# Kernel tuning notes

Hardware: AMD Instinct MI355X
Metric: run time of the kernel (lower is better)

The kernel has to match this reference:

```python
import jax, jax.numpy as jnp
import numpy as np

N_HEADS = 16
MAX_LEN = 4096
D_MODEL = 1024
EPS = 1e-6


def setup_inputs() -> dict:
    key = jax.random.key(0)
    ks = jax.random.split(key, 12)
    B, L, D = 4, 4096, D_MODEL
    s = 1.0 / np.sqrt(D)
    inp = {
        "q": jax.random.normal(ks[0], (B, L, D), jnp.float32),
        "k": jax.random.normal(ks[1], (B, L, D), jnp.float32),
        "v": jax.random.normal(ks[2], (B, L, D), jnp.float32),
        "Wq": jax.random.normal(ks[3], (D, D), jnp.float32) * s,
        "bq": jax.random.normal(ks[4], (D,), jnp.float32) * s,
        "Wk": jax.random.normal(ks[5], (D, D), jnp.float32) * s,
        "bk": jax.random.normal(ks[6], (D,), jnp.float32) * s,
        "Wv": jax.random.normal(ks[7], (D, D), jnp.float32) * s,
        "bv": jax.random.normal(ks[8], (D,), jnp.float32) * s,
        "Wo": jax.random.normal(ks[9], (D, D), jnp.float32) * s,
        "bo": jax.random.normal(ks[10], (D,), jnp.float32) * s,
    }
    return inp


def _cos_attn(q, k, v, Wq, bq, Wk, bk, Wv, bv, Wo, bo):
    B, Lq, D = q.shape
    Lk = k.shape[1]
    H = N_HEADS
    hd = D // H
    # torch Linear: x @ W^T + b
    qh = (q @ Wq.T + bq).reshape(B, Lq, H, hd).transpose(0, 2, 1, 3)  # b h l d
    kh = (k @ Wk.T + bk).reshape(B, Lk, H, hd).transpose(0, 2, 1, 3)
    vh = (v @ Wv.T + bv).reshape(B, Lk, H, hd).transpose(0, 2, 1, 3)
    qh = jax.nn.relu(qh)
    kh = jax.nn.relu(kh)
    # weight_index buffer: pi*(1..max_len)/(2*max_len), shape (1,1,L,1)
    idx = (np.pi * jnp.arange(1, MAX_LEN + 1, dtype=jnp.float32) / (2 * MAX_LEN))
    qi = idx[:Lq][None, None, :, None]
    ki = idx[:Lk][None, None, :, None]
    q_ = jnp.concatenate([qh * jnp.sin(qi), qh * jnp.cos(qi)], axis=-1)  # b h l 2d
    k_ = jnp.concatenate([kh * jnp.sin(ki), kh * jnp.cos(ki)], axis=-1)
    kv_ = jnp.einsum("bnld,bnlm->bndm", k_, vh)  # b h 2d d
    z_ = 1.0 / jnp.maximum(jnp.einsum("bnld,bnd->bnl", q_, jnp.sum(k_, axis=2)), EPS)
    attn = jnp.einsum("bnld,bndm,bnl->bnlm", q_, kv_, z_)  # b h l d
    attn = attn.transpose(0, 2, 1, 3).reshape(B, Lq, D)
    return attn @ Wo.T + bo  # dropout: eval mode (identity)


def reference(q, k, v, Wq, bq, Wk, bk, Wv, bv, Wo, bo):
    return _cos_attn(q, k, v, Wq, bq, Wk, bk, Wv, bv, Wo, bo)
```

## Files before the change

### kernel.cpp

```cpp
#include <hip/hip_runtime.h>

typedef __bf16 bf16x8 __attribute__((ext_vector_type(8)));
typedef float f32x4 __attribute__((ext_vector_type(4)));

#define PI_F 3.14159265358979323846f

__device__ __forceinline__ unsigned short f2bf(float f) {
  unsigned u = __builtin_bit_cast(unsigned, f);
  u += 0x7fffu + ((u >> 16) & 1u);
  return (unsigned short)(u >> 16);
}

__device__ __forceinline__ unsigned scale_pair(unsigned w, float f) {
  const float lo = __builtin_bit_cast(float, w << 16);
  const float hi = __builtin_bit_cast(float, w & 0xffff0000u);
  return (unsigned)f2bf(lo * f) | ((unsigned)f2bf(hi * f) << 16);
}

#define GLD16(gp, lp)                                          \
  __builtin_amdgcn_global_load_lds(                            \
      (const __attribute__((address_space(1))) void*)(gp),     \
      (__attribute__((address_space(3))) void*)(lp), 16, 0, 0)

struct AReg { float4 a0, a1, a2, a3, a4, a5, a6, a7; };

__device__ __forceinline__ uint4 cvtpk16(float4 x, float4 y) {
  unsigned c0, c1, c2, c3;
  asm("v_cvt_pk_bf16_f32 %0, %1, %2" : "=v"(c0) : "v"(x.x), "v"(x.y));
  asm("v_cvt_pk_bf16_f32 %0, %1, %2" : "=v"(c1) : "v"(x.z), "v"(x.w));
  asm("v_cvt_pk_bf16_f32 %0, %1, %2" : "=v"(c2) : "v"(y.x), "v"(y.y));
  asm("v_cvt_pk_bf16_f32 %0, %1, %2" : "=v"(c3) : "v"(y.z), "v"(y.w));
  uint4 u; u.x = c0; u.y = c1; u.z = c2; u.w = c3;
  return u;
}

__device__ __forceinline__ uint2 cvtpk8(float a, float b, float c, float d) {
  unsigned lo, hi;
  asm("v_cvt_pk_bf16_f32 %0, %1, %2" : "=v"(lo) : "v"(a), "v"(b));
  asm("v_cvt_pk_bf16_f32 %0, %1, %2" : "=v"(hi) : "v"(c), "v"(d));
  uint2 r; r.x = lo; r.y = hi;
  return r;
}

__device__ __forceinline__ void unpack8(uint4 w, float* f) {
  f[0] = __builtin_bit_cast(float, w.x << 16);
  f[1] = __builtin_bit_cast(float, w.x & 0xffff0000u);
  f[2] = __builtin_bit_cast(float, w.y << 16);
  f[3] = __builtin_bit_cast(float, w.y & 0xffff0000u);
  f[4] = __builtin_bit_cast(float, w.z << 16);
  f[5] = __builtin_bit_cast(float, w.z & 0xffff0000u);
  f[6] = __builtin_bit_cast(float, w.w << 16);
  f[7] = __builtin_bit_cast(float, w.w & 0xffff0000u);
}

__global__ __launch_bounds__(256) void convert_w(
    const float* __restrict__ Wq, const float* __restrict__ Wk,
    const float* __restrict__ Wv, const float* __restrict__ Wo,
    unsigned short* __restrict__ Wqb, unsigned short* __restrict__ Wkb,
    unsigned short* __restrict__ Wvb, unsigned short* __restrict__ Wob) {
  const int region = blockIdx.y;
  const float* s; unsigned short* d;
  switch (region) {
    case 0: s = Wq; d = Wqb; break;
    case 1: s = Wk; d = Wkb; break;
    case 2: s = Wv; d = Wvb; break;
    default: s = Wo; d = Wob; break;
  }
  const float4* s4 = (const float4*)s;
  ushort4* d4 = (ushort4*)d;
  const int n4 = 262144;
  for (int i = blockIdx.x * 256 + threadIdx.x; i < n4; i += gridDim.x * 256) {
    float4 f = s4[i];
    ushort4 o;
    o.x = f2bf(f.x); o.y = f2bf(f.y); o.z = f2bf(f.z); o.w = f2bf(f.w);
    d4[i] = o;
  }
}

template <int MODE>
__global__ __launch_bounds__(512, 2) void gemm256(
    const float* __restrict__ A32, const unsigned short* __restrict__ Bw,
    const float* __restrict__ bias, unsigned short* __restrict__ out) {
  constexpr int K = 1024, NKT = 16;
  __shared__ unsigned short S[81920];
  const int tid = threadIdx.x;
  const int wave = tid >> 6, lane = tid & 63;
  const int fr = lane & 15, fq = lane >> 4;
  const int wr = wave >> 2, wc = wave & 3;
  const int cpx = gridDim.x >> 3;
  const int wg = (blockIdx.x & 7) * cpx + (blockIdx.x >> 3);
  const int mt = wg >> 2, ntile = wg & 3;
  const int m0 = mt * 256, n0 = ntile * 256;

  const int srow = tid >> 3;
  const int ac16 = tid & 7;
  const int scolE = ((ac16 << 4) ^ ((srow & 7) << 4)) >> 1;
  const unsigned short* bSrc = Bw + (size_t)(n0 + srow) * K + scolE;
  const int awoff = (ac16 ^ (srow & 7)) << 3;
  AReg R;

#define BSTAGE(kt_, idx_) do {                                                     \
    const int kc_ = (kt_) * 64;                                                    \
    unsigned short* bb_ = S + 32768 + (idx_) * 16384 + wave * 512;                 \
    GLD16(bSrc + kc_, bb_);                                                        \
    GLD16(bSrc + (size_t)65536 + kc_, bb_ + 4096);                                 \
    GLD16(bSrc + (size_t)131072 + kc_, bb_ + 8192);                                \
    GLD16(bSrc + (size_t)196608 + kc_, bb_ + 12288);                               \
  } while (0)

#define ALOAD_ALL(kt_) do {                                                        \
    const int kc_ = (kt_) * 64;                                                    \
    const float4* p_;                                                              \
    p_ = (const float4*)(A32 + (size_t)(m0 + srow) * K + kc_) + ac16 * 2;          \
    R.a0 = p_[0]; R.a1 = p_[1];                                                    \
    p_ = (const float4*)(A32 + (size_t)(m0 + 64 + srow) * K + kc_) + ac16 * 2;     \
    R.a2 = p_[0]; R.a3 = p_[1];                                                    \
    p_ = (const float4*)(A32 + (size_t)(m0 + 128 + srow) * K + kc_) + ac16 * 2;    \
    R.a4 = p_[0]; R.a5 = p_[1];                                                    \
    p_ = (const float4*)(A32 + (size_t)(m0 + 192 + srow) * K + kc_) + ac16 * 2;    \
    R.a6 = p_[0]; R.a7 = p_[1];                                                    \
  } while (0)

#define AWRITE_ALL(idx_) do {                                                      \
    unsigned short* dst_ = &S[(idx_) * 16384 + srow * 64 + awoff];                 \
    *(uint4*)(dst_)         = cvtpk16(R.a0, R.a1);                                 \
    *(uint4*)(dst_ + 4096)  = cvtpk16(R.a2, R.a3);                                 \
    *(uint4*)(dst_ + 8192)  = cvtpk16(R.a4, R.a5);                                 \
    *(uint4*)(dst_ + 12288) = cvtpk16(R.a6, R.a7);                                 \
  } while (0)

  const int xorv = (fr & 7) << 4;
  const unsigned cbE0 = (unsigned)(((fq * 16) ^ xorv) >> 1);
  const unsigned cbE1 = (unsigned)(((64 + fq * 16) ^ xorv) >> 1);

  f32x4 acc[8][4] = {};
  ALOAD_ALL(0);
  BSTAGE(0, 0);
  BSTAGE(1, 1);
  AWRITE_ALL(0);
  ALOAD_ALL(1);
  asm volatile("s_waitcnt vmcnt(12) lgkmcnt(0)" ::: "memory");
  __builtin_amdgcn_s_barrier();

  for (int kt = 0; kt < NKT; ++kt) {
    const unsigned aB = (unsigned)((kt & 1) * 16384 + wr * 8192 + fr * 64);
    int bcur = kt % 3;
    const unsigned bB = (unsigned)(32768 + bcur * 16384 + (wc >> 1) * 8192 +
                                   ((wc & 1) * 64 + fr) * 64);
    bf16x8 af[4][2], b0[2][2], b1[2][2];
#pragma unroll
    for (int mm = 0; mm < 4; ++mm) {
      const unsigned r = aB + (unsigned)(mm * 1024);
      af[mm][0] = *(const bf16x8*)&S[r + cbE0];
      af[mm][1] = *(const bf16x8*)&S[r + cbE1];
    }
#pragma unroll
    for (int nn = 0; nn < 2; ++nn) {
      const unsigned r0 = bB + (unsigned)(nn * 1024);
      b0[nn][0] = *(const bf16x8*)&S[r0 + cbE0];
      b0[nn][1] = *(const bf16x8*)&S[r0 + cbE1];
      const unsigned r1 = bB + (unsigned)((2 + nn) * 1024);
      b1[nn][0] = *(const bf16x8*)&S[r1 + cbE0];
      b1[nn][1] = *(const bf16x8*)&S[r1 + cbE1];
    }
    if (kt + 2 < NKT) {
      int bst = bcur + 2; if (bst >= 3) bst -= 3;
      BSTAGE(kt + 2, bst);
    }
    __builtin_amdgcn_s_barrier();
    __builtin_amdgcn_s_setprio(1);
#pragma unroll
    for (int mm = 0; mm < 4; ++mm) {
#pragma unroll
      for (int nn = 0; nn < 2; ++nn) {
        acc[mm][nn] = __builtin_amdgcn_mfma_f32_16x16x32_bf16(af[mm][0], b0[nn][0], acc[mm][nn], 0, 0, 0);
        acc[mm][nn] = __builtin_amdgcn_mfma_f32_16x16x32_bf16(af[mm][1], b0[nn][1], acc[mm][nn], 0, 0, 0);
        acc[mm][2 + nn] = __builtin_amdgcn_mfma_f32_16x16x32_bf16(af[mm][0], b1[nn][0], acc[mm][2 + nn], 0, 0, 0);
        acc[mm][2 + nn] = __builtin_amdgcn_mfma_f32_16x16x32_bf16(af[mm][1], b1[nn][1], acc[mm][2 + nn], 0, 0, 0);
      }
    }
    __builtin_amdgcn_s_setprio(0);
    __builtin_amdgcn_s_barrier();
#pragma unroll
    for (int mm = 0; mm < 4; ++mm) {
      const unsigned r = aB + (unsigned)((4 + mm) * 1024);
      af[mm][0] = *(const bf16x8*)&S[r + cbE0];
      af[mm][1] = *(const bf16x8*)&S[r + cbE1];
    }
    if (kt + 1 < NKT) AWRITE_ALL((kt + 1) & 1);
    if (kt + 2 < NKT) ALOAD_ALL(kt + 2);
    __builtin_amdgcn_s_barrier();
    __builtin_amdgcn_s_setprio(1);
#pragma unroll
    for (int mm = 0; mm < 4; ++mm) {
#pragma unroll
      for (int nn = 0; nn < 2; ++nn) {
        acc[4 + mm][nn] = __builtin_amdgcn_mfma_f32_16x16x32_bf16(af[mm][0], b0[nn][0], acc[4 + mm][nn], 0, 0, 0);
        acc[4 + mm][nn] = __builtin_amdgcn_mfma_f32_16x16x32_bf16(af[mm][1], b0[nn][1], acc[4 + mm][nn], 0, 0, 0);
        acc[4 + mm][2 + nn] = __builtin_amdgcn_mfma_f32_16x16x32_bf16(af[mm][0], b1[nn][0], acc[4 + mm][2 + nn], 0, 0, 0);
        acc[4 + mm][2 + nn] = __builtin_amdgcn_mfma_f32_16x16x32_bf16(af[mm][1], b1[nn][1], acc[4 + mm][2 + nn], 0, 0, 0);
      }
    }
    __builtin_amdgcn_s_setprio(0);
    asm volatile("s_waitcnt lgkmcnt(0)" ::: "memory");
    __builtin_amdgcn_s_barrier();
  }
#undef BSTAGE
#undef ALOAD_ALL
#undef AWRITE_ALL

  const int colb = n0 + wc * 64 + fr;
  const int rtb0 = wr * 128 + fq * 4;
  const int mlo = m0 & 4095;
  const int b16 = (m0 >> 12) << 4;
  const int hbase = n0 >> 6;

  if constexpr (MODE == 0) {
    float bb4[4];
#pragma unroll
    for (int nq = 0; nq < 4; ++nq) bb4[nq] = bias[colb + nq * 16];
    __syncthreads();
#pragma unroll
    for (int mq = 0; mq < 8; ++mq) {
#pragma unroll
      for (int rr = 0; rr < 4; ++rr) {
        const int rt = rtb0 + mq * 16 + rr;
        const int e = (rt >> 2) & 7;
#pragma unroll
        for (int nq = 0; nq < 4; ++nq) {
          const int ct = wc * 64 + nq * 16 + fr;
          const int sct = (ct & 7) | ((((ct >> 3) ^ e) & 31) << 3);
          S[rt * 256 + sct] = f2bf(fmaxf(acc[mq][nq][rr] + bb4[nq], 0.0f));
        }
      }
    }
    __syncthreads();
#pragma unroll
    for (int it = 0; it < 16; ++it) {
      const int rt = it * 16 + (tid >> 5);
      const int co = tid & 31;
      const int chunk = co ^ ((rt >> 2) & 7);
      uint4 w = *(const uint4*)&S[rt * 256 + chunk * 8];
      const int h = hbase + (co >> 3);
      const size_t addr = ((size_t)(b16 + h) * 4096 + mlo + rt) * 64 + ((co & 7) << 3);
      *(uint4*)(out + addr) = w;
    }
  } else {
    float bb4[4];
#pragma unroll
    for (int nq = 0; nq < 4; ++nq) bb4[nq] = bias[colb + nq * 16];
#pragma unroll
    for (int mq = 0; mq < 8; ++mq)
#pragma unroll
      for (int nq = 0; nq < 4; ++nq)
#pragma unroll
        for (int rr = 0; rr < 4; ++rr) {
          float val = acc[mq][nq][rr] + bb4[nq];
          if constexpr (MODE == 5) val = fmaxf(val, 0.0f);
          acc[mq][nq][rr] = val;
        }
    __syncthreads();
#pragma unroll
    for (int mq = 0; mq < 8; ++mq) {
      const int rtb = rtb0 + mq * 16;
#pragma unroll
      for (int nq = 0; nq < 4; ++nq) {
        const int ct = wc * 64 + nq * 16 + fr;
        uint2 w = cvtpk8(acc[mq][nq][0], acc[mq][nq][1], acc[mq][nq][2], acc[mq][nq][3]);
        *(uint2*)&S[ct * 256 + (rtb ^ ((ct & 7) << 2))] = w;
      }
    }
    __syncthreads();
#pragma unroll
    for (int it = 0; it < 16; ++it) {
      const int ct = it * 16 + (tid >> 5);
      const int lo = (tid & 31) << 3;
      const int sw = (ct & 7) << 2;
      uint2 r0 = *(const uint2*)&S[ct * 256 + (lo ^ sw)];
      uint2 r1 = *(const uint2*)&S[ct * 256 + ((lo + 4) ^ sw)];
      uint4 w; w.x = r0.x; w.y = r0.y; w.z = r1.x; w.w = r1.y;
      const int h = hbase + (ct >> 6), dd = ct & 63;
      const size_t addr = ((size_t)(b16 + h) * 64 + dd) * 4096 + mlo + lo;
      *(uint4*)(out + addr) = w;
    }
  }
}

__global__ __launch_bounds__(512, 2) void gemm_o(
    const unsigned short* __restrict__ Ain, const unsigned short* __restrict__ Bw,
    const float* __restrict__ bias, unsigned short* __restrict__ out) {
  constexpr int K = 1024, NKT = 16;
  __shared__ unsigned short S[81920];
  const int tid = threadIdx.x;
  const int wave = tid >> 6, lane = tid & 63;
  const int fr = lane & 15, fq = lane >> 4;
  const int wr = wave >> 2, wc = wave & 3;
  const int wg = (blockIdx.x & 7) * 32 + (blockIdx.x >> 3);
  const int mt = wg >> 2, ntile = wg & 3;
  const int m0 = mt * 256, n0 = ntile * 256;

  const int srow = tid >> 3;
  const int ac16 = tid & 7;
  const int scolE = ((ac16 << 4) ^ ((srow & 7) << 4)) >> 1;
  const unsigned short* bSrc = Bw + (size_t)(n0 + srow) * K + scolE;
  const unsigned short* aSrcB = Ain + (size_t)(m0 + srow) * K + scolE;

#define BSTAGE(kt_, idx_) do {                                                     \
    const int kc_ = (kt_) * 64;                                                    \
    unsigned short* bb_ = S + 32768 + (idx_) * 16384 + wave * 512;                 \
    GLD16(bSrc + kc_, bb_);                                                        \
    GLD16(bSrc + (size_t)65536 + kc_, bb_ + 4096);                                 \
    GLD16(bSrc + (size_t)131072 + kc_, bb_ + 8192);                                \
    GLD16(bSrc + (size_t)196608 + kc_, bb_ + 12288);                               \
  } while (0)

#define ASTAGE(kt_, idx_) do {                                                     \
    const int kc_ = (kt_) * 64;                                                    \
    unsigned short* ab_ = S + (idx_) * 16384 + wave * 512;                         \
    GLD16(aSrcB + kc_, ab_);                                                       \
    GLD16(aSrcB + (size_t)65536 + kc_, ab_ + 4096);                                \
    GLD16(aSrcB + (size_t)131072 + kc_, ab_ + 8192);                               \
    GLD16(aSrcB + (size_t)196608 + kc_, ab_ + 12288);                              \
  } while (0)

  const int xorv = (fr & 7) << 4;
  const unsigned cbE0 = (unsigned)(((fq * 16) ^ xorv) >> 1);
  const unsigned cbE1 = (unsigned)(((64 + fq * 16) ^ xorv) >> 1);

  f32x4 acc[8][4] = {};
  ASTAGE(0, 0);
  BSTAGE(0, 0);
  BSTAGE(1, 1);
  asm volatile("s_waitcnt vmcnt(4)" ::: "memory");
  __builtin_amdgcn_s_barrier();

  int bcur = 0;
  for (int kt = 0; kt < NKT; ++kt) {
    const unsigned aB = (unsigned)((kt & 1) * 16384 + wr * 8192 + fr * 64);
    const unsigned bB = (unsigned)(32768 + bcur * 16384 + (wc >> 1) * 8192 +
                                   ((wc & 1) * 64 + fr) * 64);
    bf16x8 af[4][2], b0[2][2], b1[2][2];
#pragma unroll
    for (int mm = 0; mm < 4; ++mm) {
      const unsigned r = aB + (unsigned)(mm * 1024);
      af[mm][0] = *(const bf16x8*)&S[r + cbE0];
      af[mm][1] = *(const bf16x8*)&S[r + cbE1];
    }
#pragma unroll
    for (int nn = 0; nn < 2; ++nn) {
      const unsigned r0 = bB + (unsigned)(nn * 1024);
      b0[nn][0] = *(const bf16x8*)&S[r0 + cbE0];
      b0[nn][1] = *(const bf16x8*)&S[r0 + cbE1];
      const unsigned r1 = bB + (unsigned)((2 + nn) * 1024);
      b1[nn][0] = *(const bf16x8*)&S[r1 + cbE0];
      b1[nn][1] = *(const bf16x8*)&S[r1 + cbE1];
    }
    if (kt + 1 < NKT) ASTAGE(kt + 1, (kt + 1) & 1);
    if (kt + 2 < NKT) {
      int bst = bcur + 2; if (bst >= 3) bst -= 3;
      BSTAGE(kt + 2, bst);
    }
    __builtin_amdgcn_s_barrier();
    __builtin_amdgcn_s_setprio(1);
#pragma unroll
    for (int mm = 0; mm < 4; ++mm) {
#pragma unroll
      for (int nn = 0; nn < 2; ++nn) {
        acc[mm][nn] = __builtin_amdgcn_mfma_f32_16x16x32_bf16(af[mm][0], b0[nn][0], acc[mm][nn], 0, 0, 0);
        acc[mm][nn] = __builtin_amdgcn_mfma_f32_16x16x32_bf16(af[mm][1], b0[nn][1], acc[mm][nn], 0, 0, 0);
        acc[mm][2 + nn] = __builtin_amdgcn_mfma_f32_16x16x32_bf16(af[mm][0], b1[nn][0], acc[mm][2 + nn], 0, 0, 0);
        acc[mm][2 + nn] = __builtin_amdgcn_mfma_f32_16x16x32_bf16(af[mm][1], b1[nn][1], acc[mm][2 + nn], 0, 0, 0);
      }
    }
    __builtin_amdgcn_s_setprio(0);
    __builtin_amdgcn_s_barrier();
#pragma unroll
    for (int mm = 0; mm < 4; ++mm) {
      const unsigned r = aB + (unsigned)((4 + mm) * 1024);
      af[mm][0] = *(const bf16x8*)&S[r + cbE0];
      af[mm][1] = *(const bf16x8*)&S[r + cbE1];
    }
    __builtin_amdgcn_s_barrier();
    __builtin_amdgcn_s_setprio(1);
#pragma unroll
    for (int mm = 0; mm < 4; ++mm) {
#pragma unroll
      for (int nn = 0; nn < 2; ++nn) {
        acc[4 + mm][nn] = __builtin_amdgcn_mfma_f32_16x16x32_bf16(af[mm][0], b0[nn][0], acc[4 + mm][nn], 0, 0, 0);
        acc[4 + mm][nn] = __builtin_amdgcn_mfma_f32_16x16x32_bf16(af[mm][1], b0[nn][1], acc[4 + mm][nn], 0, 0, 0);
        acc[4 + mm][2 + nn] = __builtin_amdgcn_mfma_f32_16x16x32_bf16(af[mm][0], b1[nn][0], acc[4 + mm][2 + nn], 0, 0, 0);
        acc[4 + mm][2 + nn] = __builtin_amdgcn_mfma_f32_16x16x32_bf16(af[mm][1], b1[nn][1], acc[4 + mm][2 + nn], 0, 0, 0);
      }
    }
    __builtin_amdgcn_s_setprio(0);
    if (kt + 2 < NKT) {
      asm volatile("s_waitcnt vmcnt(4) lgkmcnt(0)" ::: "memory");
    } else if (kt + 1 < NKT) {
      asm volatile("s_waitcnt vmcnt(0) lgkmcnt(0)" ::: "memory");
    } else {
      asm volatile("s_waitcnt lgkmcnt(0)" ::: "memory");
    }
    __builtin_amdgcn_s_barrier();
    bcur = bcur + 1; if (bcur == 3) bcur = 0;
  }
#undef BSTAGE
#undef ASTAGE

  const int colb = n0 + wc * 64 + fr;
  float* Sf = (float*)S;
  float bb4[4];
#pragma unroll
  for (int nq = 0; nq < 4; ++nq) bb4[nq] = bias[colb + nq * 16];
  const int colL = wc * 64;
#pragma unroll
  for (int h4 = 0; h4 < 4; ++h4) {
    __syncthreads();
    if (wr == (h4 >> 1)) {
      const int mqb = (h4 & 1) * 4;
#pragma unroll
      for (int mq2 = 0; mq2 < 4; ++mq2) {
        const int rl = mq2 * 16 + fq * 4;
#pragma unroll
        for (int nq = 0; nq < 4; ++nq) {
#pragma unroll
          for (int rr = 0; rr < 4; ++rr)
            Sf[(rl + rr) * 260 + colL + nq * 16 + fr] = acc[mqb + mq2][nq][rr] + bb4[nq];
        }
      }
    }
    __syncthreads();
#pragma unroll
    for (int i = 0; i < 8; ++i) {
      const int rl = wave * 8 + i;
      const int gr = m0 + h4 * 64 + rl;
      f32x4 v4 = *(const f32x4*)&Sf[rl * 260 + lane * 4];
      uint2 w = cvtpk8(v4.x, v4.y, v4.z, v4.w);
      *(uint2*)(out + (size_t)gr * 1024 + n0 + lane * 4) = w;
    }
  }
}

__global__ __launch_bounds__(256) void expand_bf16_f32(
    const unsigned short* __restrict__ in, float* __restrict__ out) {
  const int stride = gridDim.x * 256;
  for (int i = blockIdx.x * 256 + threadIdx.x; i < 4194304; i += stride) {
    uint2 w = ((const uint2*)in)[i];
    f32x4 o;
    o.x = __builtin_bit_cast(float, w.x << 16);
    o.y = __builtin_bit_cast(float, w.x & 0xffff0000u);
    o.z = __builtin_bit_cast(float, w.y << 16);
    o.w = __builtin_bit_cast(float, w.y & 0xffff0000u);
    ((f32x4*)out)[i] = o;
  }
}

__global__ __launch_bounds__(256, 2) void kv_gemm(
    const unsigned short* __restrict__ Vt,
    const unsigned short* __restrict__ Kt,
    float* __restrict__ kvp) {
  __shared__ unsigned short As[64 * 64];
  __shared__ unsigned short Bs[128 * 64];
  __shared__ float sn[512], cn[512];
  const int tid = threadIdx.x, wave = tid >> 6, lane = tid & 63;
  const int fr = lane & 15, fq = lane >> 4;
  const int ls = blockIdx.x, bh = blockIdx.y;
  const size_t base = (size_t)bh * 64 * 4096;
  {
    float s0, c0, s1, c1;
    __sincosf(PI_F * (float)(ls * 512 + tid + 1) * (1.0f / 8192.0f), &s0, &c0);
    __sincosf(PI_F * (float)(ls * 512 + tid + 257) * (1.0f / 8192.0f), &s1, &c1);
    sn[tid] = s0; cn[tid] = c0;
    sn[tid + 256] = s1; cn[tid + 256] = c1;
  }
  f32x4 acc[5][2] = {};
  bf16x8 ones;
#pragma unroll
  for (int j = 0; j < 8; ++j) ones[j] = (__bf16)1.0f;
  for (int t = 0; t < 8; ++t) {
    const int l0 = ls * 512 + t * 64;
    __syncthreads();
#pragma unroll
    for (int j = 0; j < 2; ++j) {
      const int p = j * 256 + tid;
      const int row = p >> 3, cc = (p & 7) ^ (row & 7);
      GLD16(Vt + base + (size_t)row * 4096 + l0 + cc * 8,
            As + ((j << 8) + (wave << 6)) * 8);
    }
#pragma unroll
    for (int j = 0; j < 2; ++j) {
      const int p = j * 256 + tid;
      const int kr = p >> 3, cc = p & 7;
      const uint4 w = *(const uint4*)(Kt + base + (size_t)kr * 4096 + l0 + cc * 8);
      const int tl = t * 64 + cc * 8;
      float kf[8];
      unpack8(w, kf);
      const float4 sA = *(const float4*)&sn[tl], sB = *(const float4*)&sn[tl + 4];
      const float4 cA = *(const float4*)&cn[tl], cB = *(const float4*)&cn[tl + 4];
      float4 x0, x1;
      x0.x = kf[0] * sA.x; x0.y = kf[1] * sA.y; x0.z = kf[2] * sA.z; x0.w = kf[3] * sA.w;
      x1.x = kf[4] * sB.x; x1.y = kf[5] * sB.y; x1.z = kf[6] * sB.z; x1.w = kf[7] * sB.w;
      const uint4 wsn = cvtpk16(x0, x1);
      x0.x = kf[0] * cA.x; x0.y = kf[1] * cA.y; x0.z = kf[2] * cA.z; x0.w = kf[3] * cA.w;
      x1.x = kf[4] * cB.x; x1.y = kf[5] * cB.y; x1.z = kf[6] * cB.z; x1.w = kf[7] * cB.w;
      const uint4 wcn = cvtpk16(x0, x1);
      const int sw_ = cc ^ (kr & 7);
      *(uint4*)&Bs[(kr * 8 + sw_) * 8] = wsn;
      *(uint4*)&Bs[((kr + 64) * 8 + sw_) * 8] = wcn;
    }
    __syncthreads();
#pragma unroll
    for (int kk = 0; kk < 2; ++kk) {
      const int ch = kk * 4 + fq;
      bf16x8 a[4], b[2];
#pragma unroll
      for (int m = 0; m < 4; ++m) {
        const int r = m * 16 + fr;
        a[m] = *(const bf16x8*)&As[(r * 8 + (ch ^ (r & 7))) * 8];
      }
#pragma unroll
      for (int n = 0; n < 2; ++n) {
        const int r = wave * 32 + n * 16 + fr;
        b[n] = *(const bf16x8*)&Bs[(r * 8 + (ch ^ (r & 7))) * 8];
      }
#pragma unroll
      for (int m = 0; m < 4; ++m)
#pragma unroll
        for (int n = 0; n < 2; ++n)
          acc[m][n] = __builtin_amdgcn_mfma_f32_16x16x32_bf16(a[m], b[n], acc[m][n], 0, 0, 0);
#pragma unroll
      for (int n = 0; n < 2; ++n)
        acc[4][n] = __builtin_amdgcn_mfma_f32_16x16x32_bf16(ones, b[n], acc[4][n], 0, 0, 0);
    }
  }
  float* outp = kvp + ((size_t)bh * 8 + ls) * (65 * 128);
  const int colb = wave * 32 + fr;
#pragma unroll
  for (int n = 0; n < 2; ++n) {
    const int col = colb + n * 16;
#pragma unroll
    for (int m = 0; m < 4; ++m)
#pragma unroll
      for (int r = 0; r < 4; ++r)
        outp[(m * 16 + fq * 4 + r) * 128 + col] = acc[m][n][r];
    if (fq == 0) outp[64 * 128 + col] = acc[4][n][0];
  }
}

__global__ __launch_bounds__(256) void kv_reduce(
    const float* __restrict__ kvp, unsigned short* __restrict__ kv_ext) {
  const int bh = blockIdx.x;
  for (int e = threadIdx.x; e < 80 * 128; e += 256) {
    const int row = e >> 7, c = e & 127;
    float v = 0.0f;
    if (row < 65) {
#pragma unroll
      for (int ls = 0; ls < 8; ++ls)
        v += kvp[((size_t)bh * 8 + ls) * (65 * 128) + row * 128 + c];
    }
    kv_ext[(size_t)bh * (80 * 128) + e] = f2bf(v);
  }
}

__global__ __launch_bounds__(256) void attn_phase2(
    const unsigned short* __restrict__ Qh, const unsigned short* __restrict__ kve,
    unsigned short* __restrict__ attn) {
  __shared__ unsigned short Qs[128 * 128];
  __shared__ unsigned short Ws[80 * 128];
  const int tid = threadIdx.x, wave = tid >> 6, lane = tid & 63;
  const int fr = lane & 15, fq = lane >> 4;
  const int l0 = blockIdx.x * 128;
  const int bh = blockIdx.y, b = bh >> 4, h = bh & 15;
#pragma unroll
  for (int j = 0; j < 5; ++j) {
    const int p = j * 256 + tid;
    const int r = p >> 4, scn = p & 15;
    const int cc = scn ^ (r & 7);
    GLD16(kve + ((size_t)bh * 80 + r) * 128 + cc * 8,
          Ws + ((size_t)(j * 256 + wave * 64)) * 8);
  }
#pragma unroll
  for (int it = 0; it < 4; ++it) {
    const int qc = it * 256 + tid;
    const int r = qc >> 3, dc = qc & 7;
    const uint4 w = *(const uint4*)(Qh + ((size_t)bh * 4096 + l0 + r) * 64 + dc * 8);
    float sv, cv;
    __sincosf(PI_F * (float)(l0 + r + 1) * (1.0f / 8192.0f), &sv, &cv);
    uint4 osn, ocs;
    osn.x = scale_pair(w.x, sv); osn.y = scale_pair(w.y, sv);
    osn.z = scale_pair(w.z, sv); osn.w = scale_pair(w.w, sv);
    ocs.x = scale_pair(w.x, cv); ocs.y = scale_pair(w.y, cv);
    ocs.z = scale_pair(w.z, cv); ocs.w = scale_pair(w.w, cv);
    const int ps = r * 16 + (dc ^ (r & 7));
    *(uint4*)&Qs[ps * 8] = osn;
    *(uint4*)&Qs[(ps + 8) * 8] = ocs;
  }
  __syncthreads();
  f32x4 acc[2][5] = {};
#pragma unroll
  for (int kk = 0; kk < 4; ++kk) {
    const int cc = kk * 4 + fq;
    bf16x8 a[2], bb[5];
#pragma unroll
    for (int m = 0; m < 2; ++m) {
      const int r = wave * 32 + m * 16 + fr;
      a[m] = *(const bf16x8*)&Qs[(r * 16 + (cc ^ (r & 7))) * 8];
    }
#pragma unroll
    for (int n = 0; n < 5; ++n) {
      const int r = n * 16 + fr;
      bb[n] = *(const bf16x8*)&Ws[(r * 16 + (cc ^ (r & 7))) * 8];
    }
#pragma unroll
    for (int m = 0; m < 2; ++m)
#pragma unroll
      for (int n = 0; n < 5; ++n)
        acc[m][n] = __builtin_amdgcn_mfma_f32_16x16x32_bf16(a[m], bb[n], acc[m][n], 0, 0, 0);
  }
#pragma unroll
  for (int m = 0; m < 2; ++m) {
#pragma unroll
    for (int r = 0; r < 4; ++r) {
      const float den = __shfl(acc[m][4][r], lane & 48);
      const float z = 1.0f / fmaxf(den, 1e-6f);
      const int l = l0 + wave * 32 + m * 16 + fq * 4 + r;
      const size_t ro = ((size_t)b * 4096 + l) * 1024 + (size_t)h * 64;
#pragma unroll
      for (int n = 0; n < 4; ++n)
        attn[ro + n * 16 + fr] = f2bf(acc[m][n][r] * z);
    }
  }
}

extern "C" void kernel_launch(void* const* d_in, const int* in_sizes, int n_in,
                              void* d_out, int out_size, void* d_ws, size_t ws_size,
                              hipStream_t stream) {
  (void)in_sizes; (void)n_in; (void)out_size; (void)ws_size;
  const float* q  = (const float*)d_in[0];
  const float* k  = (const float*)d_in[1];
  const float* v  = (const float*)d_in[2];
  const float* Wq = (const float*)d_in[3];
  const float* bq = (const float*)d_in[4];
  const float* Wk = (const float*)d_in[5];
  const float* bk = (const float*)d_in[6];
  const float* Wv = (const float*)d_in[7];
  const float* bvp = (const float*)d_in[8];
  const float* Wo = (const float*)d_in[9];
  const float* bo = (const float*)d_in[10];

  char* ws = (char*)d_ws;
  unsigned short* Wqb = (unsigned short*)(ws + 0);
  unsigned short* Wkb = (unsigned short*)(ws + 2097152);
  unsigned short* Wvb = (unsigned short*)(ws + 4194304);
  unsigned short* Wob = (unsigned short*)(ws + 6291456);
  unsigned short* Qh  = (unsigned short*)(ws + 8388608);
  unsigned short* Vt  = (unsigned short*)(ws + 41943040);
  unsigned short* Kt  = (unsigned short*)(ws + 75497472);
  unsigned short* attnb = Kt;
  unsigned short* obf = Qh;
  float* kvp          = (float*)(ws + 109051904);
  unsigned short* kve = (unsigned short*)(ws + 126091264);

  convert_w<<<dim3(128, 4), 256, 0, stream>>>(Wq, Wk, Wv, Wo, Wqb, Wkb, Wvb, Wob);
  gemm256<0><<<256, 512, 0, stream>>>(q, Wqb, bq, Qh);
  gemm256<5><<<256, 512, 0, stream>>>(k, Wkb, bk, Kt);
  gemm256<4><<<256, 512, 0, stream>>>(v, Wvb, bvp, Vt);
  kv_gemm<<<dim3(8, 64), 256, 0, stream>>>(Vt, Kt, kvp);
  kv_reduce<<<64, 256, 0, stream>>>(kvp, kve);
  attn_phase2<<<dim3(32, 64), 256, 0, stream>>>(Qh, kve, attnb);
  gemm_o<<<256, 512, 0, stream>>>(attnb, Wob, bo, obf);
  expand_bf16_f32<<<2048, 256, 0, stream>>>(obf, (float*)d_out);
}
```

Baseline: 244.8 us.

## Split GEMM k-step into four MFMA phases with interleaved staging

Restructures each k-iteration of the bf16 MFMA main loop from two half-tile phases into four quarter-tile phases (two M halves by two N halves). Each phase loads its own A and B fragments from LDS, then issues one piece of the global-to-LDS staging work: the B stage, the A write, or the next A load. The goal is lower register pressure and finer interleaving of memory traffic with MFMA work. In exchange, A and B fragments are re-read from LDS twice per k-step, there are twice as many barriers, and there is a full lgkmcnt wait before every compute phase.

Result: slower. 264.2 us (+7.9%).

```diff
diff --git a/kernel.cpp b/kernel.cpp
--- a/kernel.cpp
+++ b/kernel.cpp
@@ -144,66 +144,48 @@
 
   for (int kt = 0; kt < NKT; ++kt) {
     const unsigned aB = (unsigned)((kt & 1) * 16384 + wr * 8192 + fr * 64);
-    int bcur = kt % 3;
+    const int bcur = kt % 3;
     const unsigned bB = (unsigned)(32768 + bcur * 16384 + (wc >> 1) * 8192 +
                                    ((wc & 1) * 64 + fr) * 64);
-    bf16x8 af[4][2], b0[2][2], b1[2][2];
-#pragma unroll
-    for (int mm = 0; mm < 4; ++mm) {
-      const unsigned r = aB + (unsigned)(mm * 1024);
-      af[mm][0] = *(const bf16x8*)&S[r + cbE0];
-      af[mm][1] = *(const bf16x8*)&S[r + cbE1];
-    }
-#pragma unroll
-    for (int nn = 0; nn < 2; ++nn) {
-      const unsigned r0 = bB + (unsigned)(nn * 1024);
-      b0[nn][0] = *(const bf16x8*)&S[r0 + cbE0];
-      b0[nn][1] = *(const bf16x8*)&S[r0 + cbE1];
-      const unsigned r1 = bB + (unsigned)((2 + nn) * 1024);
-      b1[nn][0] = *(const bf16x8*)&S[r1 + cbE0];
-      b1[nn][1] = *(const bf16x8*)&S[r1 + cbE1];
-    }
-    if (kt + 2 < NKT) {
-      int bst = bcur + 2; if (bst >= 3) bst -= 3;
-      BSTAGE(kt + 2, bst);
-    }
-    __builtin_amdgcn_s_barrier();
-    __builtin_amdgcn_s_setprio(1);
-#pragma unroll
-    for (int mm = 0; mm < 4; ++mm) {
+#pragma unroll
+    for (int ph = 0; ph < 4; ++ph) {
+      const int mh = ph >> 1, nh = ph & 1;
+      bf16x8 af[4][2], bfr[2][2];
+#pragma unroll
+      for (int mm = 0; mm < 4; ++mm) {
+        const unsigned r = aB + (unsigned)((mh * 4 + mm) * 1024);
+        af[mm][0] = *(const bf16x8*)&S[r + cbE0];
+        af[mm][1] = *(const bf16x8*)&S[r + cbE1];
+      }
 #pragma unroll
       for (int nn = 0; nn < 2; ++nn) {
-        acc[mm][nn] = __builtin_amdgcn_mfma_f32_16x16x32_bf16(af[mm][0], b0[nn][0], acc[mm][nn], 0, 0, 0);
-        acc[mm][nn] = __builtin_amdgcn_mfma_f32_16x16x32_bf16(af[mm][1], b0[nn][1], acc[mm][nn], 0, 0, 0);
-        acc[mm][2 + nn] = __builtin_amdgcn_mfma_f32_16x16x32_bf16(af[mm][0], b1[nn][0], acc[mm][2 + nn], 0, 0, 0);
-        acc[mm][2 + nn] = __builtin_amdgcn_mfma_f32_16x16x32_bf16(af[mm][1], b1[nn][1], acc[mm][2 + nn], 0, 0, 0);
-      }
-    }
-    __builtin_amdgcn_s_setprio(0);
-    __builtin_amdgcn_s_barrier();
-#pragma unroll
-    for (int mm = 0; mm < 4; ++mm) {
-      const unsigned r = aB + (unsigned)((4 + mm) * 1024);
-      af[mm][0] = *(const bf16x8*)&S[r + cbE0];
-      af[mm][1] = *(const bf16x8*)&S[r + cbE1];
-    }
-    if (kt + 1 < NKT) AWRITE_ALL((kt + 1) & 1);
-    if (kt + 2 < NKT) ALOAD_ALL(kt + 2);
-    __builtin_amdgcn_s_barrier();
-    __builtin_amdgcn_s_setprio(1);
-#pragma unroll
-    for (int mm = 0; mm < 4; ++mm) {
-#pragma unroll
-      for (int nn = 0; nn < 2; ++nn) {
-        acc[4 + mm][nn] = __builtin_amdgcn_mfma_f32_16x16x32_bf16(af[mm][0], b0[nn][0], acc[4 + mm][nn], 0, 0, 0);
-        acc[4 + mm][nn] = __builtin_amdgcn_mfma_f32_16x16x32_bf16(af[mm][1], b0[nn][1], acc[4 + mm][nn], 0, 0, 0);
-        acc[4 + mm][2 + nn] = __builtin_amdgcn_mfma_f32_16x16x32_bf16(af[mm][0], b1[nn][0], acc[4 + mm][2 + nn], 0, 0, 0);
-        acc[4 + mm][2 + nn] = __builtin_amdgcn_mfma_f32_16x16x32_bf16(af[mm][1], b1[nn][1], acc[4 + mm][2 + nn], 0, 0, 0);
-      }
-    }
-    __builtin_amdgcn_s_setprio(0);
-    asm volatile("s_waitcnt lgkmcnt(0)" ::: "memory");
-    __builtin_amdgcn_s_barrier();
+        const unsigned r = bB + (unsigned)((nh * 2 + nn) * 1024);
+        bfr[nn][0] = *(const bf16x8*)&S[r + cbE0];
+        bfr[nn][1] = *(const bf16x8*)&S[r + cbE1];
+      }
+      if (ph == 0 && kt + 2 < NKT) {
+        int bst = bcur + 2; if (bst >= 3) bst -= 3;
+        BSTAGE(kt + 2, bst);
+      }
+      if (ph == 1 && kt + 1 < NKT) AWRITE_ALL((kt + 1) & 1);
+      if (ph == 2 && kt + 2 < NKT) ALOAD_ALL(kt + 2);
+      __builtin_amdgcn_s_barrier();
+      asm volatile("s_waitcnt lgkmcnt(0)" ::: "memory");
+      __builtin_amdgcn_sched_barrier(0);
+      __builtin_amdgcn_s_setprio(1);
+#pragma unroll
+      for (int mm = 0; mm < 4; ++mm) {
+#pragma unroll
+        for (int nn = 0; nn < 2; ++nn) {
+          acc[mh * 4 + mm][nh * 2 + nn] = __builtin_amdgcn_mfma_f32_16x16x32_bf16(
+              af[mm][0], bfr[nn][0], acc[mh * 4 + mm][nh * 2 + nn], 0, 0, 0);
+          acc[mh * 4 + mm][nh * 2 + nn] = __builtin_amdgcn_mfma_f32_16x16x32_bf16(
+              af[mm][1], bfr[nn][1], acc[mh * 4 + mm][nh * 2 + nn], 0, 0, 0);
+        }
+      }
+      __builtin_amdgcn_s_setprio(0);
+      __builtin_amdgcn_s_barrier();
+    }
   }
 #undef BSTAGE
 #undef ALOAD_ALL
```
